# Kernel tuning notes

Measured on AMD Instinct MI355X. Metric: run time of the kernel, lower is better.

## Reference

```python
import jax, jax.numpy as jnp
import numpy as np

BETA = 0.25
K = 4096
D = 256


def setup_inputs() -> dict:
    key = jax.random.key(0)
    k1, k2 = jax.random.split(key)
    z = jax.random.normal(k1, (4, D, 16, 32, 32), dtype=jnp.float32)
    # mimics nn.init.uniform_(embed.weight, -1/K, 1/K)
    embed = jax.random.uniform(k2, (K, D), minval=-1.0 / K, maxval=1.0 / K, dtype=jnp.float32)
    return {"z": z, "embed": embed}


def reference(z, embed):
    # z: [B, D, T, H, W] -> channel-last [B, T, H, W, D]
    z_perm = jnp.transpose(z, (0, 2, 3, 4, 1))
    flat = z_perm.reshape(-1, embed.shape[1])  # [N, D]
    # squared L2 distances via expansion: |z|^2 - 2 z.e + |e|^2  -> [N, K]
    dist = ((flat ** 2).sum(axis=1, keepdims=True)
            - 2.0 * flat @ embed.T
            + (embed ** 2).sum(axis=1)[None, :])
    idx = jnp.argmin(dist, axis=1)  # [N]
    z_q = embed[idx].reshape(z_perm.shape)  # [B, T, H, W, D]
    # straight-through estimator
    z_q_st = z_perm + jax.lax.stop_gradient(z_q - z_perm)
    z_q_st = jnp.transpose(z_q_st, (0, 4, 1, 2, 3))  # back to [B, D, T, H, W]
    e_q = jnp.transpose(z_q, (0, 4, 1, 2, 3))
    codebook_loss = jnp.mean((jax.lax.stop_gradient(e_q) - z) ** 2)
    commitment_loss = jnp.mean((e_q - jax.lax.stop_gradient(z)) ** 2)
    vq_loss = codebook_loss + BETA * commitment_loss
    indices = idx.reshape(z_perm.shape[:4])  # [B, T, H, W]
    return (z_q_st, vq_loss, indices)
```

## Files before the change

kernel.cpp:

```cpp
#include <hip/hip_runtime.h>
#include <float.h>

#define KC 4096
#define DIM 256
#define MB 16384
#define NTOT 65536
#define ZELEMS 16777216
#define LOSS_OFF 16777216
#define IDX_OFF  16777217
#define TAU 1.5e-4f

#define BT_OFF   524288
#define CNT_OFF  528400
#define CAND_OFF 532480
#define FULL_OFF 800000

typedef _Float16 h8 __attribute__((ext_vector_type(8)));
typedef float f4v __attribute__((ext_vector_type(4)));

__device__ __forceinline__ bool lexlt(float av, int ai, float bv, int bi) {
    return (av < bv) || (av == bv && ai < bi);
}

__global__ __launch_bounds__(256) void vq_prep(const float* __restrict__ e,
                                               float* __restrict__ out) {
    if (blockIdx.x < 512) {
        int t = blockIdx.x * 256 + threadIdx.x;
        int code = t >> 5, s8 = t & 31;
        const float4* src = reinterpret_cast<const float4*>(e + (size_t)code * DIM + s8 * 8);
        float4 v0 = src[0], v1 = src[1];
        float f[8] = {v0.x, v0.y, v0.z, v0.w, v1.x, v1.y, v1.z, v1.w};
        union { uint4 q; _Float16 h[8]; } P;
        #pragma unroll
        for (int p = 0; p < 8; ++p) P.h[p] = (_Float16)(f[p] * 4096.0f);
        int kc = s8 >> 2, khi = s8 & 3;
        int lane = khi * 16 + (code & 15);
        int slot = ((code >> 4) * 8 + kc) * 64 + lane;
        reinterpret_cast<uint4*>(out)[slot] = P.q;
    } else {
        int k = (blockIdx.x - 512) * 4 + (threadIdx.x >> 6);
        int lane = threadIdx.x & 63;
        float4 v = reinterpret_cast<const float4*>(e + (size_t)k * DIM)[lane];
        double s = (double)v.x * v.x + (double)v.y * v.y + (double)v.z * v.z + (double)v.w * v.w;
        #pragma unroll
        for (int off = 32; off > 0; off >>= 1) s += __shfl_down(s, off);
        if (lane == 0) out[BT_OFF + k] = (float)s;
    }
}

#define INS4(V0, V1, V2, V3, L0, L1, L2, L3, v, k)                              \
    if (v < V3) {                                                               \
        if (v < V2) {                                                           \
            V3 = V2; L3 = L2;                                                   \
            if (v < V1) {                                                       \
                V2 = V1; L2 = L1;                                               \
                if (v < V0) { V1 = V0; L1 = L0; V0 = v; L0 = k; }               \
                else        { V1 = v; L1 = k; }                                 \
            } else { V2 = v; L2 = k; }                                          \
        } else { V3 = v; L3 = k; }                                              \
    }

__global__ __launch_bounds__(256) void vq_fast(const float* __restrict__ z,
                                               float* __restrict__ out) {
    __shared__ uint4 etile[2][512];
    __shared__ unsigned long long lists[4][16][4];
    const int tid = threadIdx.x;
    const int wave = tid >> 6, lane = tid & 63;
    const int khi = lane >> 4, l16 = lane & 15;
    const int nbase = blockIdx.x * 64;
    const int b = nbase / MB;
    const int mbase = nbase % MB;
    const float* zb = z + (size_t)b * DIM * MB + mbase + wave * 16 + l16;

    h8 zf[8];
    #pragma unroll
    for (int kc = 0; kc < 8; ++kc) {
        h8 va;
        #pragma unroll
        for (int j = 0; j < 8; ++j)
            va[j] = (_Float16)zb[(size_t)(kc * 32 + khi * 8 + j) * MB];
        zf[kc] = va;
    }

    const uint4* ET = reinterpret_cast<const uint4*>(out);
    const float* Btab = out + BT_OFF;

    float b1 = FLT_MAX;
    int bk = 0;
    float v0 = FLT_MAX, v1 = FLT_MAX, v2 = FLT_MAX, v3 = FLT_MAX;
    int l0 = 0, l1 = 0, l2 = 0, l3 = 0;

    uint4 r0 = ET[tid], r1 = ET[tid + 256];
    for (int tile = 0; tile < KC / 16; ++tile) {
        const int cur = tile & 1;
        etile[cur][tid] = r0; etile[cur][tid + 256] = r1;
        __syncthreads();
        if (tile < KC / 16 - 1) {
            r0 = ET[(size_t)(tile + 1) * 512 + tid];
            r1 = ET[(size_t)(tile + 1) * 512 + tid + 256];
        }

        f4v ae = {0.f, 0.f, 0.f, 0.f}, ao = ae;
        #pragma unroll
        for (int kc = 0; kc < 8; kc += 2) {
            union { uint4 q; h8 v; } afe, afo;
            afe.q = etile[cur][kc * 64 + lane];
            afo.q = etile[cur][(kc + 1) * 64 + lane];
            ae = __builtin_amdgcn_mfma_f32_16x16x32_f16(afe.v, zf[kc], ae, 0, 0, 0);
            ao = __builtin_amdgcn_mfma_f32_16x16x32_f16(afo.v, zf[kc + 1], ao, 0, 0, 0);
        }

        const f4v Bv = *reinterpret_cast<const f4v*>(Btab + tile * 16 + khi * 4);
        const int kb = tile * 16 + khi * 4;
        float sc[4];
        #pragma unroll
        for (int i = 0; i < 4; ++i)
            sc[i] = fmaf(-4.8828125e-4f, ae[i] + ao[i], Bv[i]);
        float m = fminf(fminf(sc[0], sc[1]), fminf(sc[2], sc[3]));
        if (m <= b1 + TAU) {
            #pragma unroll
            for (int i = 0; i < 4; ++i) {
                float s = sc[i]; int k = kb + i;
                if (s < b1) {
                    if (b1 <= s + TAU) INS4(v0, v1, v2, v3, l0, l1, l2, l3, b1, bk)
                    b1 = s; bk = k;
                } else if (s <= b1 + TAU) {
                    INS4(v0, v1, v2, v3, l0, l1, l2, l3, s, k)
                }
            }
        }
    }

    float gb = b1;
    int gk = bk;
    #pragma unroll
    for (int off = 16; off < 64; off <<= 1) {
        float ov = __shfl_xor(gb, off); int ok = __shfl_xor(gk, off);
        if (lexlt(ov, ok, gb, gk)) { gb = ov; gk = ok; }
    }
    const float thr = gb + TAU;

    int n = 0, pa = 0, pb = 0, pc = 0, pd = 0;
    #define ADDW(kk) { if (n == 0) pa = kk; else if (n == 1) pb = kk; \
                       else if (n == 2) pc = kk; else if (n == 3) pd = kk; n++; }
    if (b1 <= thr) ADDW(bk)
    if (v0 <= thr) ADDW(l0)
    if (v1 <= thr) ADDW(l1)
    if (v2 <= thr) ADDW(l2)
    if (v3 <= thr) ADDW(l3)
    lists[wave][l16][khi] = ((unsigned long long)n << 48) |
        (unsigned long long)pa | ((unsigned long long)pb << 12) |
        ((unsigned long long)pc << 24) | ((unsigned long long)pd << 36);
    __syncthreads();

    unsigned* cntg = (unsigned*)(out + CNT_OFF);
    {
        bool act = (lane < 16);
        int gidx = nbase + wave * 16 + l16;
        int I1 = gk;
        int tot = 0, c[4];
        c[0] = c[1] = c[2] = c[3] = I1;
        if (act) {
            #pragma unroll
            for (int q = 0; q < 4; ++q) {
                unsigned long long pl = lists[wave][l16][q];
                int pcnt = (int)(pl >> 48);
                #pragma unroll
                for (int j = 0; j < 4; ++j) {
                    int kv = (int)((pl >> (12 * j)) & 4095ull);
                    if (j < pcnt && tot + j < 4) c[tot + j] = kv;
                }
                tot += pcnt;
            }
            out[IDX_OFF + gidx] = (float)I1;
        }
        bool cand = act && (tot >= 2) && (tot <= 4);
        bool full = act && (tot > 4);
        unsigned long long mc = __ballot(cand);
        if (mc) {
            int leader = __ffsll((long long)mc) - 1;
            unsigned base = 0;
            if (lane == leader) base = atomicAdd(cntg, (unsigned)__popcll(mc));
            base = __shfl(base, leader);
            if (cand) {
                unsigned pos = base + (unsigned)__popcll(mc & ((1ull << lane) - 1ull));
                reinterpret_cast<uint4*>(out + CAND_OFF)[pos] =
                    make_uint4((unsigned)gidx,
                               (unsigned)c[0] | ((unsigned)c[1] << 16),
                               (unsigned)c[2] | ((unsigned)c[3] << 16), 0u);
            }
        }
        unsigned long long mf = __ballot(full);
        if (mf) {
            int leader = __ffsll((long long)mf) - 1;
            unsigned base = 0;
            if (lane == leader) base = atomicAdd(cntg + 1, (unsigned)__popcll(mf));
            base = __shfl(base, leader);
            if (full) {
                unsigned pos = base + (unsigned)__popcll(mf & ((1ull << lane) - 1ull));
                reinterpret_cast<unsigned*>(out + FULL_OFF)[pos] = (unsigned)gidx;
            }
        }
    }
}

__global__ __launch_bounds__(256) void vq_resolve(const float* __restrict__ z,
                                                  const float* __restrict__ e,
                                                  float* __restrict__ out) {
    __shared__ float zs[DIM];
    __shared__ float rv[4];
    __shared__ int ri[4];
    const int tid = threadIdx.x;
    const int wave = tid >> 6, lane = tid & 63;
    const float* Btab = out + BT_OFF;

    const unsigned nf = reinterpret_cast<const unsigned*>(out + CNT_OFF)[1];
    const unsigned* flist = reinterpret_cast<const unsigned*>(out + FULL_OFF);
    for (unsigned ei = blockIdx.x; ei < nf; ei += gridDim.x) {
        const int gidx = (int)flist[ei];
        const int b = gidx >> 14, m = gidx & (MB - 1);
        const float* zr = z + (size_t)b * DIM * MB + m;
        if (tid < DIM) zs[tid] = zr[(size_t)tid * MB];
        __syncthreads();
        double av = 0.0;
        #pragma unroll
        for (int t2 = 0; t2 < 4; ++t2) {
            double zv = (double)zs[lane * 4 + t2];
            av = fma(zv, zv, av);
        }
        #pragma unroll
        for (int mm = 1; mm < 64; mm <<= 1) av += __shfl_xor(av, mm);
        const float Af = (float)av;

        float bsv = FLT_MAX; int bsk = 0;
        for (int kk = 0; kk < 16; ++kk) {
            const int k = kk * 256 + tid;
            const float4* er4 = reinterpret_cast<const float4*>(e + (size_t)k * DIM);
            const float4* zs4 = reinterpret_cast<const float4*>(zs);
            double dot0 = 0.0, dot1 = 0.0;
            #pragma unroll 8
            for (int d4 = 0; d4 < 64; ++d4) {
                float4 ev = er4[d4];
                float4 zv = zs4[d4];
                dot0 = fma((double)zv.x, (double)ev.x, dot0);
                dot1 = fma((double)zv.y, (double)ev.y, dot1);
                dot0 = fma((double)zv.z, (double)ev.z, dot0);
                dot1 = fma((double)zv.w, (double)ev.w, dot1);
            }
            float s = (Af - (float)(2.0 * (dot0 + dot1))) + Btab[k];
            if (s < bsv) { bsv = s; bsk = k; }
        }
        #pragma unroll
        for (int mm = 1; mm < 64; mm <<= 1) {
            float ov = __shfl_xor(bsv, mm);
            int oi = __shfl_xor(bsk, mm);
            if (ov < bsv || (ov == bsv && oi < bsk)) { bsv = ov; bsk = oi; }
        }
        if (lane == 0) { rv[wave] = bsv; ri[wave] = bsk; }
        __syncthreads();
        if (tid == 0) {
            float bv = rv[0]; int bk = ri[0];
            #pragma unroll
            for (int wv = 1; wv < 4; ++wv) {
                if (rv[wv] < bv || (rv[wv] == bv && ri[wv] < bk)) { bv = rv[wv]; bk = ri[wv]; }
            }
            out[IDX_OFF + gidx] = (float)bk;
        }
        __syncthreads();
    }

    const unsigned nc = *reinterpret_cast<const unsigned*>(out + CNT_OFF);
    const uint4* clist = reinterpret_cast<const uint4*>(out + CAND_OFF);
    for (unsigned ei = blockIdx.x * 4 + wave; ei < nc; ei += gridDim.x * 4) {
        uint4 ent = clist[ei];
        const int gidx = (int)ent.x;
        const int c1 = (int)(ent.y & 0xFFFFu), c2 = (int)(ent.y >> 16);
        const int c3 = (int)(ent.z & 0xFFFFu), c4 = (int)(ent.z >> 16);
        const int b = gidx >> 14, m = gidx & (MB - 1);
        const float* zr = z + (size_t)b * DIM * MB + m;
        const float* e1 = e + (size_t)c1 * DIM;
        const float* e2 = e + (size_t)c2 * DIM;
        const float* e3 = e + (size_t)c3 * DIM;
        const float* e4 = e + (size_t)c4 * DIM;
        double A = 0.0;
        double d1 = 0.0, d2 = 0.0, d3 = 0.0, d4 = 0.0;
        #pragma unroll
        for (int jj = 0; jj < 4; ++jj) {
            int d = lane * 4 + jj;
            double zv = (double)zr[(size_t)d * MB];
            A = fma(zv, zv, A);
            d1 = fma(zv, (double)e1[d], d1);
            d2 = fma(zv, (double)e2[d], d2);
            d3 = fma(zv, (double)e3[d], d3);
            d4 = fma(zv, (double)e4[d], d4);
        }
        #pragma unroll
        for (int mm = 1; mm < 64; mm <<= 1) {
            A += __shfl_xor(A, mm);
            d1 += __shfl_xor(d1, mm); d2 += __shfl_xor(d2, mm);
            d3 += __shfl_xor(d3, mm); d4 += __shfl_xor(d4, mm);
        }
        if (lane == 0) {
            float Af = (float)A;
            float s1 = (Af - (float)(2.0 * d1)) + Btab[c1];
            float s2 = (Af - (float)(2.0 * d2)) + Btab[c2];
            float s3 = (Af - (float)(2.0 * d3)) + Btab[c3];
            float s4 = (Af - (float)(2.0 * d4)) + Btab[c4];
            float bv = s1; int bk = c1;
            if (lexlt(s2, c2, bv, bk)) { bv = s2; bk = c2; }
            if (lexlt(s3, c3, bv, bk)) { bv = s3; bk = c3; }
            if (lexlt(s4, c4, bv, bk)) { bv = s4; bk = c4; }
            out[IDX_OFF + gidx] = (float)bk;
        }
    }
}

__global__ __launch_bounds__(256) void vq_apply(const float* __restrict__ z,
                                                const float* __restrict__ e,
                                                float* __restrict__ out) {
    __shared__ int lds_fi[64];
    __shared__ float lds_e[64][260];
    __shared__ double lds_ls[4];
    const int tid = threadIdx.x;
    const int wave = tid >> 6, lane = tid & 63;
    const int nbase = blockIdx.x * 64;
    const int b = nbase / MB;
    const int mbase = nbase % MB;
    if (tid < 64) lds_fi[tid] = (int)out[IDX_OFF + nbase + tid];
    __syncthreads();
    for (int r = wave; r < 64; r += 4) {
        int code = lds_fi[r];
        float4 v = reinterpret_cast<const float4*>(e + (size_t)code * DIM)[lane];
        *reinterpret_cast<float4*>(&lds_e[r][lane * 4]) = v;
    }
    __syncthreads();

    double lsum = 0.0;
    const int mloc = tid & 63;
    const int d0 = tid >> 6;
    #pragma unroll 4
    for (int d = d0; d < DIM; d += 4) {
        float ev = lds_e[mloc][d];
        size_t off = (size_t)b * (DIM * MB) + (size_t)d * MB + mbase + mloc;
        float zv = z[off];
        out[off] = ev;
        float diff = ev - zv;
        lsum += (double)diff * diff;
    }
    #pragma unroll
    for (int off = 32; off > 0; off >>= 1) lsum += __shfl_down(lsum, off);
    if (lane == 0) lds_ls[wave] = lsum;
    __syncthreads();
    if (tid == 0) {
        double t = lds_ls[0] + lds_ls[1] + lds_ls[2] + lds_ls[3];
        atomicAdd(out + LOSS_OFF, (float)(t * (1.25 / (double)ZELEMS)));
    }
}

extern "C" void kernel_launch(void* const* d_in, const int* in_sizes, int n_in,
                              void* d_out, int out_size, void* d_ws, size_t ws_size,
                              hipStream_t stream) {
    const float* z = (const float*)d_in[0];
    const float* e = (const float*)d_in[1];
    float* out = (float*)d_out;

    hipMemsetAsync(out + LOSS_OFF, 0, sizeof(float), stream);
    hipMemsetAsync(out + CNT_OFF, 0, 2 * sizeof(unsigned), stream);
    vq_prep<<<1536, 256, 0, stream>>>(e, out);
    vq_fast<<<NTOT / 64, 256, 0, stream>>>(z, out);
    vq_resolve<<<1024, 256, 0, stream>>>(z, e, out);
    vq_apply<<<NTOT / 64, 256, 0, stream>>>(z, e, out);
}
```

Baseline: 427.6 us.

## Split codebook search across two blocks per row group with a merge kernel

The codebook scan in vq_fast is split in half: each 64-row group now gets two blocks, each scanning half of the codes and writing its packed near-tie candidate lists (value plus index) to a workspace region. A new vq_merge kernel combines the two halves, picks the global argmin, rebuilds the tie-candidate list and appends rows to the candidate or full-resolve queues. The aim is more parallelism and shorter per-block serial loops in the MFMA distance scan. In exchange, z is read twice, about 16MB of partial results is written and read back, and there is an extra kernel launch.

```diff
diff --git a/kernel.cpp b/kernel.cpp
--- a/kernel.cpp
+++ b/kernel.cpp
@@ -14,6 +14,7 @@
 #define CNT_OFF  528400
 #define CAND_OFF 532480
 #define FULL_OFF 800000
+#define PART_OFF 900000
 
 typedef _Float16 h8 __attribute__((ext_vector_type(8)));
 typedef float f4v __attribute__((ext_vector_type(4)));
@@ -63,11 +64,12 @@
 __global__ __launch_bounds__(256) void vq_fast(const float* __restrict__ z,
                                                float* __restrict__ out) {
     __shared__ uint4 etile[2][512];
-    __shared__ unsigned long long lists[4][16][4];
     const int tid = threadIdx.x;
     const int wave = tid >> 6, lane = tid & 63;
     const int khi = lane >> 4, l16 = lane & 15;
-    const int nbase = blockIdx.x * 64;
+    const int split = blockIdx.x & 1;
+    const int rb = blockIdx.x >> 1;
+    const int nbase = rb * 64;
     const int b = nbase / MB;
     const int mbase = nbase % MB;
     const float* zb = z + (size_t)b * DIM * MB + mbase + wave * 16 + l16;
@@ -90,12 +92,13 @@
     float v0 = FLT_MAX, v1 = FLT_MAX, v2 = FLT_MAX, v3 = FLT_MAX;
     int l0 = 0, l1 = 0, l2 = 0, l3 = 0;
 
-    uint4 r0 = ET[tid], r1 = ET[tid + 256];
-    for (int tile = 0; tile < KC / 16; ++tile) {
+    const int t0 = split * (KC / 32);
+    uint4 r0 = ET[(size_t)t0 * 512 + tid], r1 = ET[(size_t)t0 * 512 + tid + 256];
+    for (int tile = t0; tile < t0 + KC / 32; ++tile) {
         const int cur = tile & 1;
         etile[cur][tid] = r0; etile[cur][tid + 256] = r1;
         __syncthreads();
-        if (tile < KC / 16 - 1) {
+        if (tile < t0 + KC / 32 - 1) {
             r0 = ET[(size_t)(tile + 1) * 512 + tid];
             r1 = ET[(size_t)(tile + 1) * 512 + tid + 256];
         }
@@ -140,66 +143,104 @@
     }
     const float thr = gb + TAU;
 
-    int n = 0, pa = 0, pb = 0, pc = 0, pd = 0;
-    #define ADDW(kk) { if (n == 0) pa = kk; else if (n == 1) pb = kk; \
-                       else if (n == 2) pc = kk; else if (n == 3) pd = kk; n++; }
-    if (b1 <= thr) ADDW(bk)
-    if (v0 <= thr) ADDW(l0)
-    if (v1 <= thr) ADDW(l1)
-    if (v2 <= thr) ADDW(l2)
-    if (v3 <= thr) ADDW(l3)
-    lists[wave][l16][khi] = ((unsigned long long)n << 48) |
-        (unsigned long long)pa | ((unsigned long long)pb << 12) |
-        ((unsigned long long)pc << 24) | ((unsigned long long)pd << 36);
-    __syncthreads();
-
+    int n = 0;
+    unsigned long long e0 = 0, e1 = 0, e2 = 0, e3 = 0;
+    #define PUTP(vv, kk) { unsigned long long pk =                               \
+            ((unsigned long long)__float_as_uint(vv) << 32) | (unsigned)(kk);    \
+        if (n == 0) e0 = pk; else if (n == 1) e1 = pk;                           \
+        else if (n == 2) e2 = pk; else if (n == 3) e3 = pk; n++; }
+    if (b1 <= thr) PUTP(b1, bk)
+    if (v0 <= thr) PUTP(v0, l0)
+    if (v1 <= thr) PUTP(v1, l1)
+    if (v2 <= thr) PUTP(v2, l2)
+    if (v3 <= thr) PUTP(v3, l3)
+    e0 |= (unsigned long long)n << 12;
+
+    const int gidx = nbase + wave * 16 + l16;
+    unsigned long long* P = reinterpret_cast<unsigned long long*>(out + PART_OFF) +
+                            ((size_t)(split * NTOT + gidx) * 4 + khi) * 4;
+    P[0] = e0; P[1] = e1; P[2] = e2; P[3] = e3;
+}
+
+__global__ __launch_bounds__(256) void vq_merge(float* __restrict__ out) {
+    const int r = blockIdx.x * 256 + threadIdx.x;
+    const int lane = threadIdx.x & 63;
+    const unsigned long long* P = reinterpret_cast<const unsigned long long*>(out + PART_OFF);
+
+    unsigned long long ent[32];
+    int num[8];
+    #pragma unroll
+    for (int sq = 0; sq < 8; ++sq) {
+        int s = sq >> 2, q = sq & 3;
+        const unsigned long long* sub = P + ((size_t)(s * NTOT + r) * 4 + q) * 4;
+        ent[sq * 4 + 0] = sub[0]; ent[sq * 4 + 1] = sub[1];
+        ent[sq * 4 + 2] = sub[2]; ent[sq * 4 + 3] = sub[3];
+        num[sq] = (int)((ent[sq * 4] >> 12) & 7ull);
+    }
+
+    float gbv = FLT_MAX; int gbk = 0;
+    #pragma unroll
+    for (int sq = 0; sq < 8; ++sq) {
+        #pragma unroll
+        for (int j = 0; j < 4; ++j) {
+            if (j < num[sq]) {
+                unsigned long long pk = ent[sq * 4 + j];
+                float v = __uint_as_float((unsigned)(pk >> 32));
+                int k = (int)(pk & 0xFFFull);
+                if (lexlt(v, k, gbv, gbk)) { gbv = v; gbk = k; }
+            }
+        }
+    }
+    const float thr = gbv + TAU;
+    const int nt0 = num[0] + num[1] + num[2] + num[3];
+    const int nt1 = num[4] + num[5] + num[6] + num[7];
+    const bool ovf = (nt0 >= 5) || (nt1 >= 5);
+
+    int m = 0, c0 = gbk, c1 = gbk, c2 = gbk, c3 = gbk;
+    #pragma unroll
+    for (int sq = 0; sq < 8; ++sq) {
+        #pragma unroll
+        for (int j = 0; j < 4; ++j) {
+            if (j < num[sq]) {
+                unsigned long long pk = ent[sq * 4 + j];
+                float v = __uint_as_float((unsigned)(pk >> 32));
+                int k = (int)(pk & 0xFFFull);
+                if (v <= thr) {
+                    if (m == 0) c0 = k; else if (m == 1) c1 = k;
+                    else if (m == 2) c2 = k; else if (m == 3) c3 = k;
+                    m++;
+                }
+            }
+        }
+    }
+
+    out[IDX_OFF + r] = (float)gbk;
+    bool full = ovf || (m > 4);
+    bool cand = !full && (m >= 2);
     unsigned* cntg = (unsigned*)(out + CNT_OFF);
-    {
-        bool act = (lane < 16);
-        int gidx = nbase + wave * 16 + l16;
-        int I1 = gk;
-        int tot = 0, c[4];
-        c[0] = c[1] = c[2] = c[3] = I1;
-        if (act) {
-            #pragma unroll
-            for (int q = 0; q < 4; ++q) {
-                unsigned long long pl = lists[wave][l16][q];
-                int pcnt = (int)(pl >> 48);
-                #pragma unroll
-                for (int j = 0; j < 4; ++j) {
-                    int kv = (int)((pl >> (12 * j)) & 4095ull);
-                    if (j < pcnt && tot + j < 4) c[tot + j] = kv;
-                }
-                tot += pcnt;
-            }
-            out[IDX_OFF + gidx] = (float)I1;
-        }
-        bool cand = act && (tot >= 2) && (tot <= 4);
-        bool full = act && (tot > 4);
-        unsigned long long mc = __ballot(cand);
-        if (mc) {
-            int leader = __ffsll((long long)mc) - 1;
-            unsigned base = 0;
-            if (lane == leader) base = atomicAdd(cntg, (unsigned)__popcll(mc));
-            base = __shfl(base, leader);
-            if (cand) {
-                unsigned pos = base + (unsigned)__popcll(mc & ((1ull << lane) - 1ull));
-                reinterpret_cast<uint4*>(out + CAND_OFF)[pos] =
-                    make_uint4((unsigned)gidx,
-                               (unsigned)c[0] | ((unsigned)c[1] << 16),
-                               (unsigned)c[2] | ((unsigned)c[3] << 16), 0u);
-            }
-        }
-        unsigned long long mf = __ballot(full);
-        if (mf) {
-            int leader = __ffsll((long long)mf) - 1;
-            unsigned base = 0;
-            if (lane == leader) base = atomicAdd(cntg + 1, (unsigned)__popcll(mf));
-            base = __shfl(base, leader);
-            if (full) {
-                unsigned pos = base + (unsigned)__popcll(mf & ((1ull << lane) - 1ull));
-                reinterpret_cast<unsigned*>(out + FULL_OFF)[pos] = (unsigned)gidx;
-            }
+    unsigned long long mc = __ballot(cand);
+    if (mc) {
+        int leader = __ffsll((long long)mc) - 1;
+        unsigned base = 0;
+        if (lane == leader) base = atomicAdd(cntg, (unsigned)__popcll(mc));
+        base = __shfl(base, leader);
+        if (cand) {
+            unsigned pos = base + (unsigned)__popcll(mc & ((1ull << lane) - 1ull));
+            reinterpret_cast<uint4*>(out + CAND_OFF)[pos] =
+                make_uint4((unsigned)r,
+                           (unsigned)c0 | ((unsigned)c1 << 16),
+                           (unsigned)c2 | ((unsigned)c3 << 16), 0u);
+        }
+    }
+    unsigned long long mf = __ballot(full);
+    if (mf) {
+        int leader = __ffsll((long long)mf) - 1;
+        unsigned base = 0;
+        if (lane == leader) base = atomicAdd(cntg + 1, (unsigned)__popcll(mf));
+        base = __shfl(base, leader);
+        if (full) {
+            unsigned pos = base + (unsigned)__popcll(mf & ((1ull << lane) - 1ull));
+            reinterpret_cast<unsigned*>(out + FULL_OFF)[pos] = (unsigned)r;
         }
     }
 }
@@ -367,7 +408,8 @@
     hipMemsetAsync(out + LOSS_OFF, 0, sizeof(float), stream);
     hipMemsetAsync(out + CNT_OFF, 0, 2 * sizeof(unsigned), stream);
     vq_prep<<<1536, 256, 0, stream>>>(e, out);
-    vq_fast<<<NTOT / 64, 256, 0, stream>>>(z, out);
+    vq_fast<<<(NTOT / 64) * 2, 256, 0, stream>>>(z, out);
+    vq_merge<<<NTOT / 256, 256, 0, stream>>>(out);
     vq_resolve<<<1024, 256, 0, stream>>>(z, e, out);
     vq_apply<<<NTOT / 64, 256, 0, stream>>>(z, e, out);
 }
```

Result: slower. 451.9 us (+5.7%).
